# Kernel optimization log

Hardware: AMD Instinct MI355X
Metric: run time of the kernel (lower is better)

## Reference

```python
import jax, jax.numpy as jnp
import numpy as np

DPW = 1.0       # dist_push_weight
IW = 1.0        # intensity_weight
MINDIST = 0.05
MAXVAL = 255.0
KS = 11         # gaussian blur kernel size


def _gaussian_blur(img):
    """torchvision-style gaussian_blur with kernel_size=11, default sigma, reflect pad. img: [B,H,W]."""
    sigma = 0.3 * ((KS - 1) * 0.5 - 1) + 0.8  # = 2.0
    half = (KS - 1) * 0.5
    x = jnp.linspace(-half, half, KS)
    pdf = jnp.exp(-0.5 * (x / sigma) ** 2)
    k1 = (pdf / pdf.sum()).astype(img.dtype)
    pad = KS // 2
    xp = jnp.pad(img, ((0, 0), (pad, pad), (pad, pad)), mode='reflect')
    lhs = xp[:, None]  # [B,1,H+2p,W+2p]
    kh = k1.reshape(1, 1, KS, 1)
    kw = k1.reshape(1, 1, 1, KS)
    y = jax.lax.conv_general_dilated(lhs, kh, (1, 1), 'VALID')
    y = jax.lax.conv_general_dilated(y, kw, (1, 1), 'VALID')
    return y[:, 0]


def _dist_push(tr):
    """tr: [N,2]. mean over upper-triangle pairs of clamp(mindist - dist, 0)."""
    n = tr.shape[0]
    sq = jnp.sum(tr * tr, axis=-1)                       # [N]
    d2 = sq[:, None] + sq[None, :] - 2.0 * (tr @ tr.T)   # [N,N]
    d2 = jnp.maximum(d2, 0.0)
    mask = jnp.triu(jnp.ones((n, n), dtype=bool), k=1)
    d = jnp.sqrt(jnp.where(mask, d2, 1.0))               # safe sqrt off-mask
    vals = jnp.where(mask, jnp.maximum(MINDIST - d, 0.0), 0.0)
    npairs = n * (n - 1) // 2
    return jnp.sum(vals) / npairs


def _intensity(x, trace):
    """x: [H,W] blurred image, trace: [N,2] in [0,1]. Returns per-point bilinear-ish intensity [N]."""
    H, W = x.shape
    idx0 = trace[:, 0] * H
    idx1 = trace[:, 1] * W
    xp = jnp.pad(x, ((0, 2), (0, 2)), mode='reflect')    # reflect pad right/bottom by 2
    i0 = jax.lax.stop_gradient(jnp.floor(idx0 + 0.5))
    i1 = i0 + 1.0
    j0 = jax.lax.stop_gradient(jnp.floor(idx1 + 0.5))
    j1 = j0 + 1.0
    i0i = i0.astype(jnp.int32); i1i = i1.astype(jnp.int32)
    j0i = j0.astype(jnp.int32); j1i = j1.astype(jnp.int32)
    y00 = xp[i0i, j0i]
    y10 = xp[i1i, j0i]
    y01 = xp[i0i, j1i]
    out_ax0 = (i1 - idx0) * y00 + (idx0 - i0) * y10
    out_ax1 = (j1 - idx1) * y00 + (idx1 - j0) * y01
    return (out_ax0 + out_ax1) / 2.0


def setup_inputs() -> dict:
    key = jax.random.key(0)
    k1, k2 = jax.random.split(key)
    trace = jax.random.uniform(k1, (8, 4096, 2), dtype=jnp.float32)
    img = jax.random.uniform(k2, (8, 512, 512), dtype=jnp.float32)
    return {"trace": trace, "img": img}


def reference(trace, img):
    dist_push_loss = jnp.mean(jax.vmap(_dist_push)(trace))
    imgf = _gaussian_blur(img)
    intensity = jax.vmap(_intensity)(imgf, trace)   # [B,N]
    int_loss = jnp.mean(MAXVAL - intensity)
    return dist_push_loss * DPW + int_loss * IW
```

## Files before the change

### kernel.cpp

```cpp
#include <hip/hip_runtime.h>

#define IMH 512
#define IMW 512
#define NP 4096
#define NBATCH 8

__device__ constexpr float KW[11] = {
    0.00881223f, 0.02714359f, 0.06511407f, 0.12164908f, 0.17699836f,
    0.20056542f, 0.17699836f, 0.12164908f, 0.06511407f, 0.02714359f, 0.00881223f};

__device__ __forceinline__ int refl(int r) {
    r = r < 0 ? -r : r;
    return r > 511 ? 1022 - r : r;
}

__global__ __launch_bounds__(256)
void k1_dist_blur(const float* __restrict__ trace, const float* __restrict__ img,
                  float* __restrict__ ws1, float* __restrict__ accs) {
    const int tid = threadIdx.x;
    const int bx = blockIdx.x;
    if (bx < 1024) {
        __shared__ float2 pj[512];
        __shared__ float red[4];
        const int b = bx >> 7, ib = (bx >> 3) & 15, jc = bx & 7;
        const float2* tb = (const float2*)(trace + b * NP * 2);
        pj[tid] = tb[jc * 512 + tid];
        pj[tid + 256] = tb[jc * 512 + tid + 256];
        const float2 pi = tb[ib * 256 + tid];
        __syncthreads();
        float s = 0.f;
#pragma unroll 8
        for (int j = 0; j < 512; ++j) {
            float dx = pi.x - pj[j].x;
            float dy = pi.y - pj[j].y;
            float d2 = fmaf(dx, dx, dy * dy);
            s += fminf(__builtin_amdgcn_sqrtf(d2), 0.05f);
        }
        for (int o = 32; o; o >>= 1) s += __shfl_down(s, o, 64);
        if ((tid & 63) == 0) red[tid >> 6] = s;
        __syncthreads();
        if (tid == 0) atomicAdd(&accs[0], red[0] + red[1] + red[2] + red[3]);
    } else {
        const int idx = (bx - 1024) * 256 + tid;
        const int w4 = idx & 127, h = (idx >> 7) & 511, b = idx >> 16;
        const float4* ib4 = (const float4*)(img + b * (IMH * IMW));
        float4 a = make_float4(0.f, 0.f, 0.f, 0.f);
#pragma unroll
        for (int t = 0; t < 11; ++t) {
            const int r = refl(h - 5 + t);
            const float4 v = ib4[r * 128 + w4];
            a.x = fmaf(KW[t], v.x, a.x);
            a.y = fmaf(KW[t], v.y, a.y);
            a.z = fmaf(KW[t], v.z, a.z);
            a.w = fmaf(KW[t], v.w, a.w);
        }
        ((float4*)ws1)[idx] = a;
    }
}

template <bool LIGHT>
__global__ __launch_bounds__(256)
void k2_gather(const float* __restrict__ trace, const float* __restrict__ src,
               float* __restrict__ accs, unsigned* __restrict__ cnt, float* __restrict__ out) {
    const int tid = threadIdx.x;
    const int bx = blockIdx.x;
    const int b = bx >> 4;
    const int p = (bx & 15) * 256 + tid;
    const float2 t2 = ((const float2*)trace)[b * NP + p];
    const float idx0 = t2.x * 512.f, idx1 = t2.y * 512.f;
    const float i0f = floorf(idx0 + 0.5f), j0f = floorf(idx1 + 0.5f);
    const float wi = idx0 - i0f, wj = idx1 - j0f;
    const int i0 = (int)i0f, j0 = (int)j0f;
    const int mi0 = refl(i0), mi1 = refl(i0 + 1);
    const int mj0 = refl(j0), mj1 = refl(j0 + 1);
    const int ilo = min(mi0, mi1), jlo = min(mj0, mj1);
    const bool sr = mi0 > mi1, sc = mj0 > mj1;
    const float* srcb = src + b * (IMH * IMW);

    float v0[12], v1[12];
    if (LIGHT) {
        const float* r0 = srcb + mi0 * IMW;
        const float* r1 = srcb + mi1 * IMW;
#pragma unroll
        for (int c = 0; c < 12; ++c) {
            const int cc = refl(jlo - 5 + c);
            v0[c] = r0[cc];
            v1[c] = r1[cc];
        }
    } else {
        int R[12];
#pragma unroll
        for (int a = 0; a < 12; ++a) R[a] = refl(ilo - 5 + a) * IMW;
#pragma unroll
        for (int c = 0; c < 12; ++c) {
            const int cc = refl(jlo - 5 + c);
            const float* col = srcb + cc;
            float lo = 0.f, hi = 0.f;
#pragma unroll
            for (int a = 0; a < 12; ++a) {
                const float pv = col[R[a]];
                if (a < 11) lo = fmaf(KW[a], pv, lo);
                if (a > 0) hi = fmaf(KW[a - 1], pv, hi);
            }
            v0[c] = sr ? hi : lo;
            v1[c] = sr ? lo : hi;
        }
    }
    float y00lo = 0.f, y00hi = 0.f, y10lo = 0.f, y10hi = 0.f;
#pragma unroll
    for (int c = 0; c < 11; ++c) {
        y00lo = fmaf(KW[c], v0[c], y00lo);
        y00hi = fmaf(KW[c], v0[c + 1], y00hi);
        y10lo = fmaf(KW[c], v1[c], y10lo);
        y10hi = fmaf(KW[c], v1[c + 1], y10hi);
    }
    const float y00 = sc ? y00hi : y00lo;
    const float y01 = sc ? y00lo : y00hi;
    const float y10 = sc ? y10hi : y10lo;
    float s = 0.5f * ((1.f - wi) * y00 + wi * y10 + (1.f - wj) * y00 + wj * y01);

    __shared__ float red[4];
    for (int o = 32; o; o >>= 1) s += __shfl_down(s, o, 64);
    if ((tid & 63) == 0) red[tid >> 6] = s;
    __syncthreads();
    if (tid == 0) {
        atomicAdd(&accs[1], red[0] + red[1] + red[2] + red[3]);
        __threadfence();
        const unsigned o = atomicAdd(cnt, 1u);
        if (o == 127u) {
            __threadfence();
            const double M = (double)atomicAdd(&accs[0], 0.f);
            const double S1 = (double)atomicAdd(&accs[1], 0.f);
            const double dp = (6709248.0 - M) / 134184960.0;
            const double il = 255.0 - S1 / 32768.0;
            out[0] = (float)(dp + il);
        }
    }
}

extern "C" void kernel_launch(void* const* d_in, const int* in_sizes, int n_in,
                              void* d_out, int out_size, void* d_ws, size_t ws_size,
                              hipStream_t stream) {
    const float* trace = (const float*)d_in[0];
    const float* img = (const float*)d_in[1];
    float* accs = (float*)d_ws;
    unsigned* cnt = (unsigned*)((char*)d_ws + 8);
    float* ws1 = (float*)((char*)d_ws + 64);
    float* out = (float*)d_out;
    const bool light = ws_size >= (size_t)(64 + NBATCH * IMH * IMW * 4);

    hipMemsetAsync(d_ws, 0, 64, stream);
    if (light) {
        k1_dist_blur<<<3072, 256, 0, stream>>>(trace, img, ws1, accs);
        k2_gather<true><<<128, 256, 0, stream>>>(trace, ws1, accs, cnt, out);
    } else {
        k1_dist_blur<<<1024, 256, 0, stream>>>(trace, img, ws1, accs);
        k2_gather<false><<<128, 256, 0, stream>>>(trace, img, accs, cnt, out);
    }
}
```

Measured before the change: 103.8 us.

## Fuse distance-push and gather into one kernel, dropping the blur pass

The two launches (a full vertical-blur pass over the image into a workspace, then the gather kernel) are replaced by a single kernel. Gather blocks recompute the 2D blur locally from the raw image for each point, and distance blocks use smaller 256x256 tiles across 2048 blocks. The intent is to remove the full-image blur write/read and one kernel launch. In exchange each gather thread does 144 scattered loads, and gather blocks are placed first so they can overlap with the distance work.

```diff
diff --git a/kernel.cpp b/kernel.cpp
--- a/kernel.cpp
+++ b/kernel.cpp
@@ -1,9 +1,11 @@
 #include <hip/hip_runtime.h>
 
-#define IMH 512
 #define IMW 512
 #define NP 4096
-#define NBATCH 8
+
+#define GATHER_BLOCKS 128
+#define DIST_BLOCKS 2048
+#define TOTAL_BLOCKS (GATHER_BLOCKS + DIST_BLOCKS)
 
 __device__ constexpr float KW[11] = {
     0.00881223f, 0.02714359f, 0.06511407f, 0.12164908f, 0.17699836f,
@@ -15,79 +17,30 @@
 }
 
 __global__ __launch_bounds__(256)
-void k1_dist_blur(const float* __restrict__ trace, const float* __restrict__ img,
-                  float* __restrict__ ws1, float* __restrict__ accs) {
+void fused_loss(const float* __restrict__ trace, const float* __restrict__ img,
+                float* __restrict__ accs, unsigned* __restrict__ cnt, float* __restrict__ out) {
     const int tid = threadIdx.x;
     const int bx = blockIdx.x;
-    if (bx < 1024) {
-        __shared__ float2 pj[512];
-        __shared__ float red[4];
-        const int b = bx >> 7, ib = (bx >> 3) & 15, jc = bx & 7;
-        const float2* tb = (const float2*)(trace + b * NP * 2);
-        pj[tid] = tb[jc * 512 + tid];
-        pj[tid + 256] = tb[jc * 512 + tid + 256];
-        const float2 pi = tb[ib * 256 + tid];
-        __syncthreads();
-        float s = 0.f;
-#pragma unroll 8
-        for (int j = 0; j < 512; ++j) {
-            float dx = pi.x - pj[j].x;
-            float dy = pi.y - pj[j].y;
-            float d2 = fmaf(dx, dx, dy * dy);
-            s += fminf(__builtin_amdgcn_sqrtf(d2), 0.05f);
-        }
-        for (int o = 32; o; o >>= 1) s += __shfl_down(s, o, 64);
-        if ((tid & 63) == 0) red[tid >> 6] = s;
-        __syncthreads();
-        if (tid == 0) atomicAdd(&accs[0], red[0] + red[1] + red[2] + red[3]);
-    } else {
-        const int idx = (bx - 1024) * 256 + tid;
-        const int w4 = idx & 127, h = (idx >> 7) & 511, b = idx >> 16;
-        const float4* ib4 = (const float4*)(img + b * (IMH * IMW));
-        float4 a = make_float4(0.f, 0.f, 0.f, 0.f);
-#pragma unroll
-        for (int t = 0; t < 11; ++t) {
-            const int r = refl(h - 5 + t);
-            const float4 v = ib4[r * 128 + w4];
-            a.x = fmaf(KW[t], v.x, a.x);
-            a.y = fmaf(KW[t], v.y, a.y);
-            a.z = fmaf(KW[t], v.z, a.z);
-            a.w = fmaf(KW[t], v.w, a.w);
-        }
-        ((float4*)ws1)[idx] = a;
-    }
-}
+    __shared__ float2 pj[256];
+    __shared__ float red[4];
+    float local;
+    int acc_idx;
 
-template <bool LIGHT>
-__global__ __launch_bounds__(256)
-void k2_gather(const float* __restrict__ trace, const float* __restrict__ src,
-               float* __restrict__ accs, unsigned* __restrict__ cnt, float* __restrict__ out) {
-    const int tid = threadIdx.x;
-    const int bx = blockIdx.x;
-    const int b = bx >> 4;
-    const int p = (bx & 15) * 256 + tid;
-    const float2 t2 = ((const float2*)trace)[b * NP + p];
-    const float idx0 = t2.x * 512.f, idx1 = t2.y * 512.f;
-    const float i0f = floorf(idx0 + 0.5f), j0f = floorf(idx1 + 0.5f);
-    const float wi = idx0 - i0f, wj = idx1 - j0f;
-    const int i0 = (int)i0f, j0 = (int)j0f;
-    const int mi0 = refl(i0), mi1 = refl(i0 + 1);
-    const int mj0 = refl(j0), mj1 = refl(j0 + 1);
-    const int ilo = min(mi0, mi1), jlo = min(mj0, mj1);
-    const bool sr = mi0 > mi1, sc = mj0 > mj1;
-    const float* srcb = src + b * (IMH * IMW);
+    if (bx < GATHER_BLOCKS) {
+        const int b = bx >> 4;
+        const int p = (bx & 15) * 256 + tid;
+        const float2 t2 = ((const float2*)trace)[b * NP + p];
+        const float idx0 = t2.x * 512.f, idx1 = t2.y * 512.f;
+        const float i0f = floorf(idx0 + 0.5f), j0f = floorf(idx1 + 0.5f);
+        const float wi = idx0 - i0f, wj = idx1 - j0f;
+        const int i0 = (int)i0f, j0 = (int)j0f;
+        const int mi0 = refl(i0), mi1 = refl(i0 + 1);
+        const int mj0 = refl(j0), mj1 = refl(j0 + 1);
+        const int ilo = min(mi0, mi1), jlo = min(mj0, mj1);
+        const bool sr = mi0 > mi1, sc = mj0 > mj1;
+        const float* srcb = img + b * (IMW * IMW);
 
-    float v0[12], v1[12];
-    if (LIGHT) {
-        const float* r0 = srcb + mi0 * IMW;
-        const float* r1 = srcb + mi1 * IMW;
-#pragma unroll
-        for (int c = 0; c < 12; ++c) {
-            const int cc = refl(jlo - 5 + c);
-            v0[c] = r0[cc];
-            v1[c] = r1[cc];
-        }
-    } else {
+        float v0[12], v1[12];
         int R[12];
 #pragma unroll
         for (int a = 0; a < 12; ++a) R[a] = refl(ilo - 5 + a) * IMW;
@@ -105,29 +58,46 @@
             v0[c] = sr ? hi : lo;
             v1[c] = sr ? lo : hi;
         }
+        float y00lo = 0.f, y00hi = 0.f, y10lo = 0.f, y10hi = 0.f;
+#pragma unroll
+        for (int c = 0; c < 11; ++c) {
+            y00lo = fmaf(KW[c], v0[c], y00lo);
+            y00hi = fmaf(KW[c], v0[c + 1], y00hi);
+            y10lo = fmaf(KW[c], v1[c], y10lo);
+            y10hi = fmaf(KW[c], v1[c + 1], y10hi);
+        }
+        const float y00 = sc ? y00hi : y00lo;
+        const float y01 = sc ? y00lo : y00hi;
+        const float y10 = sc ? y10hi : y10lo;
+        local = 0.5f * ((1.f - wi) * y00 + wi * y10 + (1.f - wj) * y00 + wj * y01);
+        acc_idx = 1;
+    } else {
+        const int d = bx - GATHER_BLOCKS;
+        const int b = d >> 8, ib = (d >> 4) & 15, jc = d & 15;
+        const float2* tb = (const float2*)(trace + b * NP * 2);
+        const float2 pi = tb[ib * 256 + tid];
+        pj[tid] = tb[jc * 256 + tid];
+        __syncthreads();
+        float s = 0.f;
+#pragma unroll 8
+        for (int j = 0; j < 256; ++j) {
+            const float dx = pi.x - pj[j].x;
+            const float dy = pi.y - pj[j].y;
+            const float d2 = fmaf(dx, dx, dy * dy);
+            s += fminf(__builtin_amdgcn_sqrtf(d2), 0.05f);
+        }
+        local = s;
+        acc_idx = 0;
     }
-    float y00lo = 0.f, y00hi = 0.f, y10lo = 0.f, y10hi = 0.f;
-#pragma unroll
-    for (int c = 0; c < 11; ++c) {
-        y00lo = fmaf(KW[c], v0[c], y00lo);
-        y00hi = fmaf(KW[c], v0[c + 1], y00hi);
-        y10lo = fmaf(KW[c], v1[c], y10lo);
-        y10hi = fmaf(KW[c], v1[c + 1], y10hi);
-    }
-    const float y00 = sc ? y00hi : y00lo;
-    const float y01 = sc ? y00lo : y00hi;
-    const float y10 = sc ? y10hi : y10lo;
-    float s = 0.5f * ((1.f - wi) * y00 + wi * y10 + (1.f - wj) * y00 + wj * y01);
 
-    __shared__ float red[4];
-    for (int o = 32; o; o >>= 1) s += __shfl_down(s, o, 64);
-    if ((tid & 63) == 0) red[tid >> 6] = s;
+    for (int o = 32; o; o >>= 1) local += __shfl_down(local, o, 64);
+    if ((tid & 63) == 0) red[tid >> 6] = local;
     __syncthreads();
     if (tid == 0) {
-        atomicAdd(&accs[1], red[0] + red[1] + red[2] + red[3]);
+        atomicAdd(&accs[acc_idx], red[0] + red[1] + red[2] + red[3]);
         __threadfence();
         const unsigned o = atomicAdd(cnt, 1u);
-        if (o == 127u) {
+        if (o == TOTAL_BLOCKS - 1) {
             __threadfence();
             const double M = (double)atomicAdd(&accs[0], 0.f);
             const double S1 = (double)atomicAdd(&accs[1], 0.f);
@@ -145,16 +115,8 @@
     const float* img = (const float*)d_in[1];
     float* accs = (float*)d_ws;
     unsigned* cnt = (unsigned*)((char*)d_ws + 8);
-    float* ws1 = (float*)((char*)d_ws + 64);
     float* out = (float*)d_out;
-    const bool light = ws_size >= (size_t)(64 + NBATCH * IMH * IMW * 4);
 
     hipMemsetAsync(d_ws, 0, 64, stream);
-    if (light) {
-        k1_dist_blur<<<3072, 256, 0, stream>>>(trace, img, ws1, accs);
-        k2_gather<true><<<128, 256, 0, stream>>>(trace, ws1, accs, cnt, out);
-    } else {
-        k1_dist_blur<<<1024, 256, 0, stream>>>(trace, img, ws1, accs);
-        k2_gather<false><<<128, 256, 0, stream>>>(trace, img, accs, cnt, out);
-    }
+    fused_loss<<<TOTAL_BLOCKS, 256, 0, stream>>>(trace, img, accs, cnt, out);
 }
```

Measured after the change: 166.7 us. 60.7% more time.
